# Kernel optimization log

Hardware: AMD Instinct MI355X
Metric: run time of the kernel (lower is better)

## Reference

```python
import math
import jax, jax.numpy as jnp
import numpy as np

H = 16  # num_heads

def get_alibi_slopes(n):
    def pow2_slopes(n):
        start = 2 ** (-2 ** (-(math.log2(n) - 3)))
        return [start * start ** i for i in range(n)]
    if math.log2(n).is_integer():
        return pow2_slopes(n)
    c = 2 ** math.floor(math.log2(n))
    return pow2_slopes(c) + get_alibi_slopes(2 * c)[0::2][: n - c]

def alibi_bias(num_heads, L, dtype=jnp.float32):
    slopes = jnp.asarray(get_alibi_slopes(num_heads), dtype=dtype)  # [H]
    pos = jnp.arange(L)
    rel = (pos[None, :] - pos[:, None]).astype(dtype)               # [L, L] = x - y
    bias = slopes[:, None, None] * rel[None, :, :]                  # [H, L, L]
    causal = pos[None, :] <= pos[:, None]                           # tril mask
    return jnp.where(causal[None, :, :], bias, -jnp.inf)


def setup_inputs() -> dict:
    key = jax.random.key(0)
    ks = jax.random.split(key, 4)
    D = 1024
    B, L = 2, 2048
    s_in = 1.0 / math.sqrt(D)
    return {
        "x": jax.random.normal(ks[0], (B, L, D), dtype=jnp.float32),
        "w_in": jax.random.normal(ks[1], (D, 3 * D), dtype=jnp.float32) * s_in,
        "b_in": jnp.zeros((3 * D,), dtype=jnp.float32),
        "w_out": jax.random.normal(ks[2], (D, D), dtype=jnp.float32) * s_in,
        "b_out": jnp.zeros((D,), dtype=jnp.float32),
    }


def reference(x, w_in, b_in, w_out, b_out):
    B, L, D = x.shape
    dh = D // H
    qkv = x @ w_in + b_in                                   # [B, L, 3D]
    q, k, v = jnp.split(qkv, 3, axis=-1)
    # [B, L, D] -> [B, H, L, dh]
    def heads(t):
        return t.reshape(B, L, H, dh).transpose(0, 2, 1, 3)
    q, k, v = heads(q), heads(k), heads(v)
    scores = jnp.einsum("bhqd,bhkd->bhqk", q, k) / math.sqrt(dh)
    scores = scores + alibi_bias(H, L, scores.dtype)[None]  # [B, H, L, L]
    attn = jax.nn.softmax(scores, axis=-1)
    out = jnp.einsum("bhqk,bhkd->bhqd", attn, v)            # [B, H, L, dh]
    out = out.transpose(0, 2, 1, 3).reshape(B, L, D)
    return out @ w_out + b_out
```

## Files before the change

### kernel.cpp

```cpp
#include <hip/hip_runtime.h>
#include <stdint.h>
#include <math.h>

#define NH 16
#define DH 64
#define SEQ 2048
#define DMODEL 1024

typedef short short8 __attribute__((ext_vector_type(8)));
typedef short short4v __attribute__((ext_vector_type(4)));
typedef float f32x4 __attribute__((ext_vector_type(4)));
typedef __bf16 bf16x4 __attribute__((ext_vector_type(4)));

__device__ __forceinline__ short f2bf(float f) {
  __bf16 h = (__bf16)f;
  return __builtin_bit_cast(short, h);
}
__device__ __forceinline__ short4v cvt4(f32x4 v) {
  bf16x4 b = __builtin_convertvector(v, bf16x4);
  return __builtin_bit_cast(short4v, b);
}
__device__ __forceinline__ float fast_exp2(float x) {
#if __has_builtin(__builtin_amdgcn_exp2f)
  return __builtin_amdgcn_exp2f(x);
#else
  return exp2f(x);
#endif
}

typedef const __attribute__((address_space(1))) uint32_t* gp_t;
typedef __attribute__((address_space(3))) uint32_t* lp_t;
__device__ __forceinline__ void async16(const short* g, short* l) {
  __builtin_amdgcn_global_load_lds((gp_t)g, (lp_t)l, 16, 0, 0);
}

__device__ __forceinline__ void transpose_tile(const float* __restrict__ in,
                                               short* __restrict__ out, int R, int C,
                                               int t, int tilesX, int tid) {
  __shared__ float tile[32][33];
  const int tx = tid & 31, ty = tid >> 5;
  const int c0 = (t % tilesX) * 32, r0 = (t / tilesX) * 32;
#pragma unroll
  for (int i = 0; i < 4; ++i)
    tile[ty + i * 8][tx] = in[(size_t)(r0 + ty + i * 8) * C + c0 + tx];
  __syncthreads();
#pragma unroll
  for (int i = 0; i < 4; ++i)
    out[(size_t)(c0 + ty + i * 8) * R + r0 + tx] = f2bf(tile[tx][ty + i * 8]);
}

__global__ void k_prep(const float* __restrict__ x, short* __restrict__ xb,
                       const float* __restrict__ w_in, short* __restrict__ w_in_t,
                       const float* __restrict__ w_out, short* __restrict__ w_out_t) {
  const int tid = threadIdx.x;
  const int blk = blockIdx.x;
  if (blk < 4096) {
    const int i = blk * 256 + tid;
    f32x4 v = ((const f32x4*)x)[i];
    ((short4v*)xb)[i] = cvt4(v);
  } else if (blk < 4096 + 3072) {
    transpose_tile(w_in, w_in_t, 1024, 3072, blk - 4096, 96, tid);
  } else {
    transpose_tile(w_out, w_out_t, 1024, 1024, blk - 7168, 32, tid);
  }
}

template <int MODE>
__launch_bounds__(256, 3)
__global__ void k_gemm(const short* __restrict__ A, const short* __restrict__ Bt,
                       const float* __restrict__ bias, float* __restrict__ Cf,
                       short* __restrict__ qo, short* __restrict__ ko,
                       short* __restrict__ vo) {
  constexpr int KD = 1024;
  __shared__ __align__(16) short As[128 * 64];
  __shared__ __align__(16) short Bs[128 * 64];
  const int tid = threadIdx.x;
  const int wave = tid >> 6, lane = tid & 63;
  const int quad = lane >> 4, l16 = lane & 15;
  const int wm = wave >> 1, wn = wave & 1;
  const int tM = blockIdx.y * 128, tN = blockIdx.x * 128;

  const short* pA[4];
  const short* pB[4];
  short* lA[4];
  short* lB[4];
#pragma unroll
  for (int t = 0; t < 4; ++t) {
    const int c = t * 256 + tid;
    const int row = c >> 3, gch = (c & 7) ^ (row & 7);
    pA[t] = A + (size_t)(tM + row) * KD + gch * 8;
    pB[t] = Bt + (size_t)(tN + row) * KD + gch * 8;
    lA[t] = &As[c * 8];
    lB[t] = &Bs[c * 8];
  }

  const int sw = l16 & 7;
  const int col0 = (quad ^ sw) << 3;
  const int col1 = col0 ^ 32;

  f32x4 acc[4][4] = {};

  for (int k0 = 0; k0 < KD; k0 += 64) {
    __syncthreads();
#pragma unroll
    for (int t = 0; t < 4; ++t) {
      async16(pA[t] + k0, lA[t]);
      async16(pB[t] + k0, lB[t]);
    }
    __syncthreads();
#pragma unroll
    for (int kh = 0; kh < 2; ++kh) {
      const int col = kh ? col1 : col0;
      short8 af[4], bfr[4];
#pragma unroll
      for (int i = 0; i < 4; ++i)
        af[i] = *(const short8*)&As[(wm * 64 + i * 16 + l16) * 64 + col];
#pragma unroll
      for (int i = 0; i < 4; ++i)
        bfr[i] = *(const short8*)&Bs[(wn * 64 + i * 16 + l16) * 64 + col];
#pragma unroll
      for (int i = 0; i < 4; ++i)
#pragma unroll
        for (int j = 0; j < 4; ++j)
          acc[i][j] = __builtin_amdgcn_mfma_f32_16x16x32_bf16(af[i], bfr[j], acc[i][j], 0, 0, 0);
    }
  }

  const int rbase = tM + wm * 64 + quad * 4;
#pragma unroll
  for (int i = 0; i < 4; ++i) {
#pragma unroll
    for (int j = 0; j < 4; ++j) {
      const int col = tN + wn * 64 + j * 16 + l16;
      const float bi = bias[col];
      if (MODE == 0) {
        const int which = col >> 10;
        const int h = (col & 1023) >> 6, d = col & 63;
        if (which == 2) {
          const int row0 = rbase + i * 16;
          const int b = row0 >> 11, li0 = row0 & 2047;
          f32x4 t;
#pragma unroll
          for (int rr = 0; rr < 4; ++rr) t[rr] = acc[i][j][rr] + bi;
          *(short4v*)&vo[(((size_t)(b * NH + h)) * DH + d) * SEQ + li0] = cvt4(t);
        } else {
          short* dst = (which == 0) ? qo : ko;
#pragma unroll
          for (int rr = 0; rr < 4; ++rr) {
            const int row = rbase + i * 16 + rr;
            const int b = row >> 11, li = row & 2047;
            dst[(((size_t)(b * NH + h)) * SEQ + li) * DH + d] = f2bf(acc[i][j][rr] + bi);
          }
        }
      } else {
#pragma unroll
        for (int rr = 0; rr < 4; ++rr) {
          const int row = rbase + i * 16 + rr;
          Cf[(size_t)row * DMODEL + col] = acc[i][j][rr] + bi;
        }
      }
    }
  }
}

__launch_bounds__(256)
__global__ void k_attn(const short* __restrict__ q, const short* __restrict__ k,
                       const short* __restrict__ vt, short* __restrict__ o) {
  __shared__ __align__(16) short Ks[2][64 * 64];
  __shared__ __align__(16) short Vs[2][64 * 64];
  __shared__ __align__(16) short Ps[4][16 * 64];
  const int tid = threadIdx.x;
  const int wave = tid >> 6, lane = tid & 63;
  const int quad = lane >> 4, l16 = lane & 15;
  const int sw = l16 & 7;
  const int qt = 31 - (blockIdx.x >> 5);
  const int bh = blockIdx.x & 31;
  const int h = bh & (NH - 1);
  const size_t base = (size_t)bh * SEQ * DH;
  const float LOG2E = 1.44269504088896f;
  const float slope2 = exp2f(-0.5f * (float)(h + 1)) * LOG2E;
  const float scale2 = 0.125f * LOG2E;
  const float FM = 12.0f;

  const int c0i = tid, c1i = 256 + tid;
  const int r0 = c0i >> 3, ch0 = (c0i & 7) ^ (r0 & 7);
  const int r1 = c1i >> 3, ch1 = (c1i & 7) ^ (r1 & 7);
  const int qk_off0 = r0 * DH + ch0 * 8;
  const int qk_off1 = r1 * DH + ch1 * 8;
  const int v_off0 = r0 * SEQ + ch0 * 8;
  const int v_off1 = r1 * SEQ + ch1 * 8;

  const int col0 = ((quad ^ sw) << 3);
  const int col1 = col0 ^ 32;
  int psoff[4];
#pragma unroll
  for (int in = 0; in < 4; ++in)
    psoff[in] = l16 * 64 + (((2 * in + (quad >> 1)) ^ sw) << 3) + (quad & 1) * 4;
  const int qlim4 = wave * 16 + l16 - 4 * quad;

  const int q0 = qt * 64;
  const int qrow = q0 + wave * 16 + l16;
  const short* qp = q + base + (size_t)qrow * DH + quad * 8;
  const short8 qb0 = *(const short8*)qp;
  const short8 qb1 = *(const short8*)(qp + 32);

  short8 ones;
#pragma unroll
  for (int j = 0; j < 8; ++j) ones[j] = (short)0x3F80;

  f32x4 accO[4] = {};
  f32x4 accL = {};
  const float qoff = -slope2 * (float)qrow - FM + slope2 * (float)(4 * quad);
  float inoff[4];
#pragma unroll
  for (int in = 0; in < 4; ++in)
    inoff[in] = qoff + slope2 * (float)(16 * in);
  const float s64 = slope2 * 64.0f;
  float rc[4];
#pragma unroll
  for (int r = 0; r < 4; ++r) rc[r] = slope2 * (float)r;

  const short* kp = k + base;
  const short* vp = vt + base;

  async16(kp + qk_off0, &Ks[0][c0i * 8]);
  async16(kp + qk_off1, &Ks[0][c1i * 8]);
  async16(vp + v_off0, &Vs[0][c0i * 8]);
  async16(vp + v_off1, &Vs[0][c1i * 8]);
  kp += 64 * DH;
  vp += 64;
  __syncthreads();

  for (int kt = 0; kt <= qt; ++kt) {
    const int cur = kt & 1, nxt = cur ^ 1;
    if (kt < qt) {
      async16(kp + qk_off0, &Ks[nxt][c0i * 8]);
      async16(kp + qk_off1, &Ks[nxt][c1i * 8]);
      async16(vp + v_off0, &Vs[nxt][c0i * 8]);
      async16(vp + v_off1, &Vs[nxt][c1i * 8]);
      kp += 64 * DH;
      vp += 64;
    }

    f32x4 s[4];
#pragma unroll
    for (int in = 0; in < 4; ++in) {
      const short8 ka0 = *(const short8*)&Ks[cur][(in * 16 + l16) * 64 + col0];
      const short8 ka1 = *(const short8*)&Ks[cur][(in * 16 + l16) * 64 + col1];
      f32x4 t = {};
      t = __builtin_amdgcn_mfma_f32_16x16x32_bf16(ka0, qb0, t, 0, 0, 0);
      t = __builtin_amdgcn_mfma_f32_16x16x32_bf16(ka1, qb1, t, 0, 0, 0);
      s[in] = t;
    }

    if (kt == qt) {
#pragma unroll
      for (int in = 0; in < 4; ++in) {
        f32x4 p;
#pragma unroll
        for (int r = 0; r < 4; ++r) {
          float val = fast_exp2(fmaf(s[in][r], scale2, inoff[in] + rc[r]));
          p[r] = (16 * in + r <= qlim4) ? val : 0.f;
        }
        *(short4v*)&Ps[wave][psoff[in]] = cvt4(p);
      }
    } else {
#pragma unroll
      for (int in = 0; in < 4; ++in) {
        f32x4 p;
#pragma unroll
        for (int r = 0; r < 4; ++r)
          p[r] = fast_exp2(fmaf(s[in][r], scale2, inoff[in] + rc[r]));
        *(short4v*)&Ps[wave][psoff[in]] = cvt4(p);
      }
    }
#pragma unroll
    for (int in = 0; in < 4; ++in) inoff[in] += s64;

    const short8 pa0 = *(const short8*)&Ps[wave][l16 * 64 + col0];
    const short8 pa1 = *(const short8*)&Ps[wave][l16 * 64 + col1];
    accL = __builtin_amdgcn_mfma_f32_16x16x32_bf16(ones, pa0, accL, 0, 0, 0);
    accL = __builtin_amdgcn_mfma_f32_16x16x32_bf16(ones, pa1, accL, 0, 0, 0);
#pragma unroll
    for (int i = 0; i < 4; ++i) {
      const short8 va0 = *(const short8*)&Vs[cur][(i * 16 + l16) * 64 + col0];
      const short8 va1 = *(const short8*)&Vs[cur][(i * 16 + l16) * 64 + col1];
      accO[i] = __builtin_amdgcn_mfma_f32_16x16x32_bf16(va0, pa0, accO[i], 0, 0, 0);
      accO[i] = __builtin_amdgcn_mfma_f32_16x16x32_bf16(va1, pa1, accO[i], 0, 0, 0);
    }
    __syncthreads();
  }

  const float inv = 1.0f / accL[0];
  const int b = bh >> 4;
  short* ob = o + ((((size_t)b * SEQ + qrow) * NH + h) * DH + 4 * quad);
#pragma unroll
  for (int i = 0; i < 4; ++i) {
    f32x4 t;
#pragma unroll
    for (int r = 0; r < 4; ++r) t[r] = accO[i][r] * inv;
    *(short4v*)&ob[16 * i] = cvt4(t);
  }
}

extern "C" void kernel_launch(void* const* d_in, const int* in_sizes, int n_in,
                              void* d_out, int out_size, void* d_ws, size_t ws_size,
                              hipStream_t stream) {
  const float* x = (const float*)d_in[0];
  const float* w_in = (const float*)d_in[1];
  const float* b_in = (const float*)d_in[2];
  const float* w_out = (const float*)d_in[3];
  const float* b_out = (const float*)d_in[4];
  float* out = (float*)d_out;

  char* ws = (char*)d_ws;
  short* xb = (short*)(ws);
  short* w_in_t = (short*)(ws + (8u << 20));
  short* w_out_t = (short*)(ws + (14u << 20));
  short* qv = (short*)(ws + (16u << 20));
  short* kv = (short*)(ws + (24u << 20));
  short* vv = (short*)(ws + (32u << 20));
  short* ao = (short*)(ws + (40u << 20));

  k_prep<<<8192, 256, 0, stream>>>(x, xb, w_in, w_in_t, w_out, w_out_t);
  k_gemm<0><<<dim3(24, 32), 256, 0, stream>>>(xb, w_in_t, b_in, nullptr, qv, kv, vv);
  k_attn<<<1024, 256, 0, stream>>>(qv, kv, vv, ao);
  k_gemm<1><<<dim3(8, 32), 256, 0, stream>>>(ao, w_out_t, b_out, out, nullptr, nullptr, nullptr);
}
```

Baseline: 169.1 us.

## Process two query tiles per attention block to reuse K/V loads

Each attention block now handles 128 query rows, as two 64-row groups per wave, instead of 64. K and V tiles loaded into shared memory are reused across both groups, which halves K/V global traffic and the block count. The grid order is remapped so that long and short causal blocks interleave for load balance. In exchange the kernel uses more registers and shared memory for P, which may lower occupancy.

Result: slower. 181.0 us (+7.1%).

```diff
diff --git a/kernel.cpp b/kernel.cpp
--- a/kernel.cpp
+++ b/kernel.cpp
@@ -168,13 +168,14 @@
                        const short* __restrict__ vt, short* __restrict__ o) {
   __shared__ __align__(16) short Ks[2][64 * 64];
   __shared__ __align__(16) short Vs[2][64 * 64];
-  __shared__ __align__(16) short Ps[4][16 * 64];
+  __shared__ __align__(16) short Ps[4][32 * 64];
   const int tid = threadIdx.x;
   const int wave = tid >> 6, lane = tid & 63;
   const int quad = lane >> 4, l16 = lane & 15;
   const int sw = l16 & 7;
-  const int qt = 31 - (blockIdx.x >> 5);
-  const int bh = blockIdx.x & 31;
+  const int bx = blockIdx.x;
+  const int qt2 = (bx < 256) ? (15 - (bx >> 5)) : ((bx - 256) >> 5);
+  const int bh = bx & 31;
   const int h = bh & (NH - 1);
   const size_t base = (size_t)bh * SEQ * DH;
   const float LOG2E = 1.44269504088896f;
@@ -192,30 +193,33 @@
 
   const int col0 = ((quad ^ sw) << 3);
   const int col1 = col0 ^ 32;
-  int psoff[4];
+  int pscol[4];
 #pragma unroll
   for (int in = 0; in < 4; ++in)
-    psoff[in] = l16 * 64 + (((2 * in + (quad >> 1)) ^ sw) << 3) + (quad & 1) * 4;
+    pscol[in] = (((2 * in + (quad >> 1)) ^ sw) << 3) + (quad & 1) * 4;
   const int qlim4 = wave * 16 + l16 - 4 * quad;
 
-  const int q0 = qt * 64;
-  const int qrow = q0 + wave * 16 + l16;
-  const short* qp = q + base + (size_t)qrow * DH + quad * 8;
-  const short8 qb0 = *(const short8*)qp;
-  const short8 qb1 = *(const short8*)(qp + 32);
+  const int q0 = qt2 * 128;
+  const int qrow0 = q0 + wave * 16 + l16;
+  short8 qbA[2], qbB[2];
+#pragma unroll
+  for (int g = 0; g < 2; ++g) {
+    const short* qp = q + base + (size_t)(qrow0 + 64 * g) * DH + quad * 8;
+    qbA[g] = *(const short8*)qp;
+    qbB[g] = *(const short8*)(qp + 32);
+  }
 
   short8 ones;
 #pragma unroll
   for (int j = 0; j < 8; ++j) ones[j] = (short)0x3F80;
 
-  f32x4 accO[4] = {};
-  f32x4 accL = {};
-  const float qoff = -slope2 * (float)qrow - FM + slope2 * (float)(4 * quad);
+  f32x4 accO[2][4] = {};
+  f32x4 accL[2] = {};
+  const float s64 = slope2 * 64.0f;
   float inoff[4];
 #pragma unroll
   for (int in = 0; in < 4; ++in)
-    inoff[in] = qoff + slope2 * (float)(16 * in);
-  const float s64 = slope2 * 64.0f;
+    inoff[in] = slope2 * (float)(16 * in + 4 * quad) - slope2 * (float)qrow0 - FM;
   float rc[4];
 #pragma unroll
   for (int r = 0; r < 4; ++r) rc[r] = slope2 * (float)r;
@@ -231,9 +235,12 @@
   vp += 64;
   __syncthreads();
 
-  for (int kt = 0; kt <= qt; ++kt) {
+  const int ktdiag = 2 * qt2;
+  const int ktlast = 2 * qt2 + 1;
+
+  for (int kt = 0; kt <= ktlast; ++kt) {
     const int cur = kt & 1, nxt = cur ^ 1;
-    if (kt < qt) {
+    if (kt < ktlast) {
       async16(kp + qk_off0, &Ks[nxt][c0i * 8]);
       async16(kp + qk_off1, &Ks[nxt][c1i * 8]);
       async16(vp + v_off0, &Vs[nxt][c0i * 8]);
@@ -242,64 +249,88 @@
       vp += 64;
     }
 
-    f32x4 s[4];
+    short8 ka[8];
 #pragma unroll
     for (int in = 0; in < 4; ++in) {
-      const short8 ka0 = *(const short8*)&Ks[cur][(in * 16 + l16) * 64 + col0];
-      const short8 ka1 = *(const short8*)&Ks[cur][(in * 16 + l16) * 64 + col1];
-      f32x4 t = {};
-      t = __builtin_amdgcn_mfma_f32_16x16x32_bf16(ka0, qb0, t, 0, 0, 0);
-      t = __builtin_amdgcn_mfma_f32_16x16x32_bf16(ka1, qb1, t, 0, 0, 0);
-      s[in] = t;
-    }
-
-    if (kt == qt) {
+      ka[2 * in] = *(const short8*)&Ks[cur][(in * 16 + l16) * 64 + col0];
+      ka[2 * in + 1] = *(const short8*)&Ks[cur][(in * 16 + l16) * 64 + col1];
+    }
+
+#pragma unroll
+    for (int g = 0; g < 2; ++g) {
+      if (g == 0 && kt == ktlast) continue;
+      f32x4 s[4];
 #pragma unroll
       for (int in = 0; in < 4; ++in) {
-        f32x4 p;
-#pragma unroll
-        for (int r = 0; r < 4; ++r) {
-          float val = fast_exp2(fmaf(s[in][r], scale2, inoff[in] + rc[r]));
-          p[r] = (16 * in + r <= qlim4) ? val : 0.f;
+        f32x4 t = {};
+        t = __builtin_amdgcn_mfma_f32_16x16x32_bf16(ka[2 * in], qbA[g], t, 0, 0, 0);
+        t = __builtin_amdgcn_mfma_f32_16x16x32_bf16(ka[2 * in + 1], qbB[g], t, 0, 0, 0);
+        s[in] = t;
+      }
+      const float gadj = g ? -s64 : 0.0f;
+      const bool diag = (g == 0) ? (kt == ktdiag) : (kt == ktlast);
+      const int psrow = (g * 16 + l16) * 64;
+      if (diag) {
+#pragma unroll
+        for (int in = 0; in < 4; ++in) {
+          f32x4 p;
+#pragma unroll
+          for (int r = 0; r < 4; ++r) {
+            float val = fast_exp2(fmaf(s[in][r], scale2, inoff[in] + rc[r] + gadj));
+            p[r] = (16 * in + r <= qlim4) ? val : 0.f;
+          }
+          *(short4v*)&Ps[wave][psrow + pscol[in]] = cvt4(p);
         }
-        *(short4v*)&Ps[wave][psoff[in]] = cvt4(p);
+      } else {
+#pragma unroll
+        for (int in = 0; in < 4; ++in) {
+          f32x4 p;
+#pragma unroll
+          for (int r = 0; r < 4; ++r)
+            p[r] = fast_exp2(fmaf(s[in][r], scale2, inoff[in] + rc[r] + gadj));
+          *(short4v*)&Ps[wave][psrow + pscol[in]] = cvt4(p);
+        }
       }
-    } else {
-#pragma unroll
-      for (int in = 0; in < 4; ++in) {
-        f32x4 p;
-#pragma unroll
-        for (int r = 0; r < 4; ++r)
-          p[r] = fast_exp2(fmaf(s[in][r], scale2, inoff[in] + rc[r]));
-        *(short4v*)&Ps[wave][psoff[in]] = cvt4(p);
-      }
     }
 #pragma unroll
     for (int in = 0; in < 4; ++in) inoff[in] += s64;
 
-    const short8 pa0 = *(const short8*)&Ps[wave][l16 * 64 + col0];
-    const short8 pa1 = *(const short8*)&Ps[wave][l16 * 64 + col1];
-    accL = __builtin_amdgcn_mfma_f32_16x16x32_bf16(ones, pa0, accL, 0, 0, 0);
-    accL = __builtin_amdgcn_mfma_f32_16x16x32_bf16(ones, pa1, accL, 0, 0, 0);
+    short8 pa[2][2];
+#pragma unroll
+    for (int g = 0; g < 2; ++g) {
+      if (g == 0 && kt == ktlast) continue;
+      pa[g][0] = *(const short8*)&Ps[wave][(g * 16 + l16) * 64 + col0];
+      pa[g][1] = *(const short8*)&Ps[wave][(g * 16 + l16) * 64 + col1];
+      accL[g] = __builtin_amdgcn_mfma_f32_16x16x32_bf16(ones, pa[g][0], accL[g], 0, 0, 0);
+      accL[g] = __builtin_amdgcn_mfma_f32_16x16x32_bf16(ones, pa[g][1], accL[g], 0, 0, 0);
+    }
 #pragma unroll
     for (int i = 0; i < 4; ++i) {
       const short8 va0 = *(const short8*)&Vs[cur][(i * 16 + l16) * 64 + col0];
       const short8 va1 = *(const short8*)&Vs[cur][(i * 16 + l16) * 64 + col1];
-      accO[i] = __builtin_amdgcn_mfma_f32_16x16x32_bf16(va0, pa0, accO[i], 0, 0, 0);
-      accO[i] = __builtin_amdgcn_mfma_f32_16x16x32_bf16(va1, pa1, accO[i], 0, 0, 0);
+#pragma unroll
+      for (int g = 0; g < 2; ++g) {
+        if (g == 0 && kt == ktlast) continue;
+        accO[g][i] = __builtin_amdgcn_mfma_f32_16x16x32_bf16(va0, pa[g][0], accO[g][i], 0, 0, 0);
+        accO[g][i] = __builtin_amdgcn_mfma_f32_16x16x32_bf16(va1, pa[g][1], accO[g][i], 0, 0, 0);
+      }
     }
     __syncthreads();
   }
 
-  const float inv = 1.0f / accL[0];
   const int b = bh >> 4;
-  short* ob = o + ((((size_t)b * SEQ + qrow) * NH + h) * DH + 4 * quad);
-#pragma unroll
-  for (int i = 0; i < 4; ++i) {
-    f32x4 t;
-#pragma unroll
-    for (int r = 0; r < 4; ++r) t[r] = accO[i][r] * inv;
-    *(short4v*)&ob[16 * i] = cvt4(t);
+#pragma unroll
+  for (int g = 0; g < 2; ++g) {
+    const float inv = 1.0f / accL[g][0];
+    const int qrow = qrow0 + 64 * g;
+    short* ob = o + ((((size_t)b * SEQ + qrow) * NH + h) * DH + 4 * quad);
+#pragma unroll
+    for (int i = 0; i < 4; ++i) {
+      f32x4 t;
+#pragma unroll
+      for (int r = 0; r < 4; ++r) t[r] = accO[g][i][r] * inv;
+      *(short4v*)&ob[16 * i] = cvt4(t);
+    }
   }
 }
 
@@ -324,6 +355,6 @@
 
   k_prep<<<8192, 256, 0, stream>>>(x, xb, w_in, w_in_t, w_out, w_out_t);
   k_gemm<0><<<dim3(24, 32), 256, 0, stream>>>(xb, w_in_t, b_in, nullptr, qv, kv, vv);
-  k_attn<<<1024, 256, 0, stream>>>(qv, kv, vv, ao);
+  k_attn<<<512, 256, 0, stream>>>(qv, kv, vv, ao);
   k_gemm<1><<<dim3(8, 32), 256, 0, stream>>>(ao, w_out_t, b_out, out, nullptr, nullptr, nullptr);
 }
```

## Split attention key tiles across waves and reduce partial outputs in shared memory

Applied to the files above, without the earlier changes.

Each wave now handles a 16-key slice of every 64-key tile for all 64 query rows, instead of 16 query rows against all keys. This lets P be fed straight from registers into 16x16x16 MFMAs without the LDS round-trip and removes the ones-matrix MFMA for the row sum. The cost is a serialized cross-wave reduction of accO and lsum through shared memory at the end, plus more accumulator registers. Launch bounds are set to target three blocks per CU.

After: 170.3 us. No clear change (+0.7%).

```diff
diff --git a/kernel.cpp b/kernel.cpp
--- a/kernel.cpp
+++ b/kernel.cpp
@@ -25,6 +25,15 @@
   return __builtin_amdgcn_exp2f(x);
 #else
   return exp2f(x);
+#endif
+}
+
+__device__ __forceinline__ f32x4 mfma16(short4v a, short4v b, f32x4 c) {
+#if __has_builtin(__builtin_amdgcn_mfma_f32_16x16x16bf16_1k)
+  return __builtin_amdgcn_mfma_f32_16x16x16bf16_1k(a, b, c, 0, 0, 0);
+#else
+  asm volatile("v_mfma_f32_16x16x16_bf16 %0, %1, %2, %0" : "+v"(c) : "v"(a), "v"(b));
+  return c;
 #endif
 }
 
@@ -163,12 +172,11 @@
   }
 }
 
-__launch_bounds__(256)
+__launch_bounds__(256, 3)
 __global__ void k_attn(const short* __restrict__ q, const short* __restrict__ k,
                        const short* __restrict__ vt, short* __restrict__ o) {
   __shared__ __align__(16) short Ks[2][64 * 64];
   __shared__ __align__(16) short Vs[2][64 * 64];
-  __shared__ __align__(16) short Ps[4][16 * 64];
   const int tid = threadIdx.x;
   const int wave = tid >> 6, lane = tid & 63;
   const int quad = lane >> 4, l16 = lane & 15;
@@ -190,35 +198,33 @@
   const int v_off0 = r0 * SEQ + ch0 * 8;
   const int v_off1 = r1 * SEQ + ch1 * 8;
 
-  const int col0 = ((quad ^ sw) << 3);
-  const int col1 = col0 ^ 32;
-  int psoff[4];
-#pragma unroll
-  for (int in = 0; in < 4; ++in)
-    psoff[in] = l16 * 64 + (((2 * in + (quad >> 1)) ^ sw) << 3) + (quad & 1) * 4;
-  const int qlim4 = wave * 16 + l16 - 4 * quad;
+  const int krow = (16 * wave + l16) * 64;
+  const int kcol0 = (quad ^ sw) << 3;
+  const int kcol1 = kcol0 ^ 32;
+  const int vcol = (((2 * wave + (quad >> 1)) ^ sw) << 3) + (quad & 1) * 4;
 
   const int q0 = qt * 64;
-  const int qrow = q0 + wave * 16 + l16;
-  const short* qp = q + base + (size_t)qrow * DH + quad * 8;
-  const short8 qb0 = *(const short8*)qp;
-  const short8 qb1 = *(const short8*)(qp + 32);
-
-  short8 ones;
-#pragma unroll
-  for (int j = 0; j < 8; ++j) ones[j] = (short)0x3F80;
-
-  f32x4 accO[4] = {};
-  f32x4 accL = {};
-  const float qoff = -slope2 * (float)qrow - FM + slope2 * (float)(4 * quad);
-  float inoff[4];
-#pragma unroll
-  for (int in = 0; in < 4; ++in)
-    inoff[in] = qoff + slope2 * (float)(16 * in);
+  short8 qf0[4], qf1[4];
+#pragma unroll
+  for (int g = 0; g < 4; ++g) {
+    const short* qp = q + base + (size_t)(q0 + 16 * g + l16) * DH + quad * 8;
+    qf0[g] = *(const short8*)qp;
+    qf1[g] = *(const short8*)(qp + 32);
+  }
+
+  f32x4 accO[4][4] = {};
+  float lsum[4] = {0.f, 0.f, 0.f, 0.f};
+
+  float kb_r[4];
+#pragma unroll
+  for (int r = 0; r < 4; ++r)
+    kb_r[r] = slope2 * (float)(16 * wave + 4 * quad + r) - FM;
+  float gq[4];
+#pragma unroll
+  for (int g = 0; g < 4; ++g)
+    gq[g] = -slope2 * (float)(q0 + 16 * g + l16);
   const float s64 = slope2 * 64.0f;
-  float rc[4];
-#pragma unroll
-  for (int r = 0; r < 4; ++r) rc[r] = slope2 * (float)r;
+  const int keybase = 16 * wave + 4 * quad;
 
   const short* kp = k + base;
   const short* vp = vt + base;
@@ -242,64 +248,99 @@
       vp += 64;
     }
 
-    f32x4 s[4];
-#pragma unroll
-    for (int in = 0; in < 4; ++in) {
-      const short8 ka0 = *(const short8*)&Ks[cur][(in * 16 + l16) * 64 + col0];
-      const short8 ka1 = *(const short8*)&Ks[cur][(in * 16 + l16) * 64 + col1];
-      f32x4 t = {};
-      t = __builtin_amdgcn_mfma_f32_16x16x32_bf16(ka0, qb0, t, 0, 0, 0);
-      t = __builtin_amdgcn_mfma_f32_16x16x32_bf16(ka1, qb1, t, 0, 0, 0);
-      s[in] = t;
-    }
-
-    if (kt == qt) {
-#pragma unroll
-      for (int in = 0; in < 4; ++in) {
-        f32x4 p;
+    const short8 ka0 = *(const short8*)&Ks[cur][krow + kcol0];
+    const short8 ka1 = *(const short8*)&Ks[cur][krow + kcol1];
+    short4v va[4];
+#pragma unroll
+    for (int i = 0; i < 4; ++i)
+      va[i] = *(const short4v*)&Vs[cur][(16 * i + l16) * 64 + vcol];
+
+    const bool diag = (kt == qt);
+#pragma unroll
+    for (int g = 0; g < 4; ++g) {
+      f32x4 s = {};
+      s = __builtin_amdgcn_mfma_f32_16x16x32_bf16(ka0, qf0[g], s, 0, 0, 0);
+      s = __builtin_amdgcn_mfma_f32_16x16x32_bf16(ka1, qf1[g], s, 0, 0, 0);
+      f32x4 p;
+      if (diag) {
+        const int qloc = 16 * g + l16;
 #pragma unroll
         for (int r = 0; r < 4; ++r) {
-          float val = fast_exp2(fmaf(s[in][r], scale2, inoff[in] + rc[r]));
-          p[r] = (16 * in + r <= qlim4) ? val : 0.f;
+          float val = fast_exp2(fmaf(s[r], scale2, kb_r[r] + gq[g]));
+          p[r] = (keybase + r <= qloc) ? val : 0.f;
         }
-        *(short4v*)&Ps[wave][psoff[in]] = cvt4(p);
-      }
-    } else {
-#pragma unroll
-      for (int in = 0; in < 4; ++in) {
-        f32x4 p;
+      } else {
 #pragma unroll
         for (int r = 0; r < 4; ++r)
-          p[r] = fast_exp2(fmaf(s[in][r], scale2, inoff[in] + rc[r]));
-        *(short4v*)&Ps[wave][psoff[in]] = cvt4(p);
-      }
-    }
-#pragma unroll
-    for (int in = 0; in < 4; ++in) inoff[in] += s64;
-
-    const short8 pa0 = *(const short8*)&Ps[wave][l16 * 64 + col0];
-    const short8 pa1 = *(const short8*)&Ps[wave][l16 * 64 + col1];
-    accL = __builtin_amdgcn_mfma_f32_16x16x32_bf16(ones, pa0, accL, 0, 0, 0);
-    accL = __builtin_amdgcn_mfma_f32_16x16x32_bf16(ones, pa1, accL, 0, 0, 0);
-#pragma unroll
-    for (int i = 0; i < 4; ++i) {
-      const short8 va0 = *(const short8*)&Vs[cur][(i * 16 + l16) * 64 + col0];
-      const short8 va1 = *(const short8*)&Vs[cur][(i * 16 + l16) * 64 + col1];
-      accO[i] = __builtin_amdgcn_mfma_f32_16x16x32_bf16(va0, pa0, accO[i], 0, 0, 0);
-      accO[i] = __builtin_amdgcn_mfma_f32_16x16x32_bf16(va1, pa1, accO[i], 0, 0, 0);
-    }
+          p[r] = fast_exp2(fmaf(s[r], scale2, kb_r[r] + gq[g]));
+      }
+      lsum[g] += p[0] + p[1] + p[2] + p[3];
+      const short4v pb = cvt4(p);
+#pragma unroll
+      for (int i = 0; i < 4; ++i) accO[g][i] = mfma16(va[i], pb, accO[g][i]);
+    }
+#pragma unroll
+    for (int r = 0; r < 4; ++r) kb_r[r] += s64;
     __syncthreads();
   }
 
-  const float inv = 1.0f / accL[0];
-  const int b = bh >> 4;
-  short* ob = o + ((((size_t)b * SEQ + qrow) * NH + h) * DH + 4 * quad);
-#pragma unroll
-  for (int i = 0; i < 4; ++i) {
-    f32x4 t;
-#pragma unroll
-    for (int r = 0; r < 4; ++r) t[r] = accO[i][r] * inv;
-    *(short4v*)&ob[16 * i] = cvt4(t);
+  f32x4* rb4 = (f32x4*)&Ks[0][0];
+  float* lb = (float*)&Vs[0][0];
+  if (wave == 0) {
+#pragma unroll
+    for (int g = 0; g < 4; ++g) {
+#pragma unroll
+      for (int i = 0; i < 4; ++i) rb4[(g * 4 + i) * 64 + lane] = accO[g][i];
+      lb[g * 64 + lane] = lsum[g];
+    }
+  }
+  __syncthreads();
+  if (wave == 1) {
+#pragma unroll
+    for (int g = 0; g < 4; ++g) {
+#pragma unroll
+      for (int i = 0; i < 4; ++i) {
+        accO[g][i] += rb4[(g * 4 + i) * 64 + lane];
+        rb4[(g * 4 + i) * 64 + lane] = accO[g][i];
+      }
+      lsum[g] += lb[g * 64 + lane];
+      lb[g * 64 + lane] = lsum[g];
+    }
+  }
+  __syncthreads();
+  if (wave == 2) {
+#pragma unroll
+    for (int g = 0; g < 4; ++g) {
+#pragma unroll
+      for (int i = 0; i < 4; ++i) {
+        accO[g][i] += rb4[(g * 4 + i) * 64 + lane];
+        rb4[(g * 4 + i) * 64 + lane] = accO[g][i];
+      }
+      lsum[g] += lb[g * 64 + lane];
+      lb[g * 64 + lane] = lsum[g];
+    }
+  }
+  __syncthreads();
+  if (wave == 3) {
+    const int b = bh >> 4;
+#pragma unroll
+    for (int g = 0; g < 4; ++g) {
+#pragma unroll
+      for (int i = 0; i < 4; ++i) accO[g][i] += rb4[(g * 4 + i) * 64 + lane];
+      lsum[g] += lb[g * 64 + lane];
+      lsum[g] += __shfl_xor(lsum[g], 16, 64);
+      lsum[g] += __shfl_xor(lsum[g], 32, 64);
+      const float inv = 1.0f / lsum[g];
+      const int qrow = q0 + 16 * g + l16;
+      short* ob = o + (((size_t)b * SEQ + qrow) * NH + h) * DH + 4 * quad;
+#pragma unroll
+      for (int i = 0; i < 4; ++i) {
+        f32x4 t;
+#pragma unroll
+        for (int r = 0; r < 4; ++r) t[r] = accO[g][i][r] * inv;
+        *(short4v*)&ob[16 * i] = cvt4(t);
+      }
+    }
   }
 }
 
```
